# Kernel optimization log

Measured on AMD Instinct MI355X. Metric: run time of the kernel, lower is better.

The kernel has to match this reference:

```python
import jax, jax.numpy as jnp
import numpy as np

D = 28            # matrix_dim = sqrt(word_emb_dim) = sqrt(784)
EMB = D * D       # 784
N_WORDS = 32000


def setup_inputs() -> dict:
    key = jax.random.key(0)
    k1, k2 = jax.random.split(key)
    eye_flat = jnp.eye(D, dtype=jnp.float32).reshape(-1)
    # 'identity' init strategy: N(0, 0.1) + identity on the diagonal
    table = jax.random.normal(k1, (N_WORDS + 1, EMB), dtype=jnp.float32) * 0.1 + eye_flat
    # row 0 is the neutral element (padding) = identity matrix
    table = table.at[0].set(eye_flat)
    sent = jax.random.randint(k2, (2048, 64), 0, N_WORDS + 1, dtype=jnp.int32)
    return {"table": table, "sent": sent}


def reference(table, sent):
    B, S = sent.shape
    # embedding gather -> per-word matrices [B, S, D, D]
    mats = table[sent].reshape(B, S, D, D)
    # continual multiplication: cur = M_0 @ M_1 @ ... @ M_{S-1}
    def step(cur, m):  # cur: [B, D, D], m: [B, D, D]
        return jnp.matmul(cur, m), None
    rest = jnp.moveaxis(mats[:, 1:], 1, 0)  # [S-1, B, D, D]
    out, _ = jax.lax.scan(step, mats[:, 0], rest)
    return out.reshape(B, EMB)
```

## Files before the change

### kernel.cpp

```cpp
#include <hip/hip_runtime.h>
#include <stdint.h>


#define D 28
#define EMB 784
#define SEQ 64
#define NITEMS 2048
#define LPI 7
#define IPW 9
#define RPL 4
#define NCHUNK 28
#define CHUNK_F 256
#define BUF_F (NCHUNK * CHUNK_F)

typedef __attribute__((address_space(3))) uint32_t lds_u32;
typedef const __attribute__((address_space(1))) uint32_t glb_u32;

__device__ __forceinline__ void dma_mat(const float* glane, float* lds0) {
#pragma unroll
  for (int t = 0; t < NCHUNK; ++t)
    __builtin_amdgcn_global_load_lds((glb_u32*)(glane + t * D),
                                     (lds_u32*)(lds0 + t * CHUNK_F), 16, 0, 0);
}

#define MATMUL(Aa, Cc)                                                         \
  do {                                                                         \
    _Pragma("unroll") for (int k = 0; k < D; ++k) {                            \
      _Pragma("unroll") for (int jv = 0; jv < 7; ++jv) {                       \
        float4 m = *(const float4*)(Bs + k * CHUNK_F + 4 * jv);                \
        _Pragma("unroll") for (int r = 0; r < RPL; ++r) {                      \
          float a = Aa[r][k];                                                  \
          if (k == 0) {                                                        \
            Cc[r][4 * jv + 0] = a * m.x;                                       \
            Cc[r][4 * jv + 1] = a * m.y;                                       \
            Cc[r][4 * jv + 2] = a * m.z;                                       \
            Cc[r][4 * jv + 3] = a * m.w;                                       \
          } else {                                                             \
            Cc[r][4 * jv + 0] = fmaf(a, m.x, Cc[r][4 * jv + 0]);               \
            Cc[r][4 * jv + 1] = fmaf(a, m.y, Cc[r][4 * jv + 1]);               \
            Cc[r][4 * jv + 2] = fmaf(a, m.z, Cc[r][4 * jv + 2]);               \
            Cc[r][4 * jv + 3] = fmaf(a, m.w, Cc[r][4 * jv + 3]);               \
          }                                                                    \
        }                                                                      \
      }                                                                        \
    }                                                                          \
  } while (0)

#define STEP(Aa, Cc)                                                           \
  do {                                                                         \
    __builtin_amdgcn_s_waitcnt(0x0f70);           \
    __syncthreads();                                                           \
    MATMUL(Aa, Cc);                                                            \
    __syncthreads();               \
    if (s + 1 < SEG_LEN) {                                                     \
      dma_mat(gn, lds);                                                        \
      int nn = (s + 2 < SEG_LEN) ? s + 2 : SEG_LEN - 1;                        \
      gn = glane(nn);                                                          \
    }                                                                          \
    ++s;                                                                       \
  } while (0)

template <int SEG_LEN, int PSEG, bool GATHER>
__global__ __launch_bounds__(64, 1) void chain_kernel(
    const float* __restrict__ src, const int* __restrict__ sent,
    float* __restrict__ dst, int ntask) {
  __shared__ __align__(16) float lds[BUF_F];

  const int lane = threadIdx.x;
  int slot = lane / LPI;
  int rl = lane - slot * LPI;
  if (slot >= IPW) { slot = IPW - 1; rl = LPI - 1; }
  int task = blockIdx.x * IPW + slot;
  if (task >= ntask) task = ntask - 1;

  const int* sp = nullptr;
  if (GATHER) {
    const int item = task / PSEG;
    const int seg = task - item * PSEG;
    sp = sent + item * SEQ + seg * SEG_LEN;
  }
  auto glane = [&](int s) -> const float* {
    const float* m = GATHER ? src + (size_t)sp[s] * EMB
                            : src + ((size_t)task * SEG_LEN + s) * EMB;
    return m + rl * 4;
  };

  float A0[RPL][D], A1[RPL][D];

  {
    const float* m0 = GATHER ? src + (size_t)sp[0] * EMB
                             : src + (size_t)task * SEG_LEN * EMB;
#pragma unroll
    for (int r = 0; r < RPL; ++r) {
      const float* rp = m0 + (rl * RPL + r) * D;
#pragma unroll
      for (int jv = 0; jv < 7; ++jv) {
        float4 v = *(const float4*)(rp + 4 * jv);
        A0[r][4 * jv + 0] = v.x;
        A0[r][4 * jv + 1] = v.y;
        A0[r][4 * jv + 2] = v.z;
        A0[r][4 * jv + 3] = v.w;
      }
    }
  }

  dma_mat(glane(1), lds);
  const float* gn = glane(SEG_LEN > 2 ? 2 : 1);
  const float* Bs = lds + slot * (LPI * 4);

  int s = 1;
#pragma unroll 1
  for (int p = 0; p < (SEG_LEN - 1) / 2; ++p) {
    STEP(A0, A1);
    STEP(A1, A0);
  }
  STEP(A0, A1);

  {
    float* op = dst + (size_t)task * EMB;
#pragma unroll
    for (int r = 0; r < RPL; ++r) {
      float* rp = op + (rl * RPL + r) * D;
#pragma unroll
      for (int jv = 0; jv < 7; ++jv) {
        *(float4*)(rp + 4 * jv) =
            make_float4(A1[r][4 * jv + 0], A1[r][4 * jv + 1],
                        A1[r][4 * jv + 2], A1[r][4 * jv + 3]);
      }
    }
  }
}

extern "C" void kernel_launch(void* const* d_in, const int* in_sizes, int n_in,
                              void* d_out, int out_size, void* d_ws, size_t ws_size,
                              hipStream_t stream) {
  const float* table = (const float*)d_in[0];
  const int* sent = (const int*)d_in[1];
  float* out = (float*)d_out;

  const size_t need = (size_t)NITEMS * 4 * EMB * sizeof(float);
  if (ws_size >= need) {
    float* p = (float*)d_ws;
    const int ntask1 = NITEMS * 4;
    chain_kernel<16, 4, true><<<(ntask1 + IPW - 1) / IPW, 64, 0, stream>>>(
        table, sent, p, ntask1);
    chain_kernel<4, 1, false><<<(NITEMS + IPW - 1) / IPW, 64, 0, stream>>>(
        p, nullptr, out, NITEMS);
  } else {
    chain_kernel<64, 1, true><<<(NITEMS + IPW - 1) / IPW, 64, 0, stream>>>(
        table, sent, out, NITEMS);
  }
}
```

Baseline: 261.6 us.

## Fuse segment chain and combine stages into one kernel via LDS exchange

Replaces the two-kernel scheme (16-length segment products written to workspace, then a second kernel combining four segments) with one kernel. Each wavefront now handles two items of four segments each (8 slots instead of 9). Segments 1-3 write their partial products into LDS, and slots 0 and 4 multiply them in to produce the final result directly. This removes the workspace round-trip and the second launch, but the full-chain fallback path is dropped, lane 63 is left idle, and most slots sit idle during the final three serial matmuls.

```diff
diff --git a/kernel.cpp b/kernel.cpp
--- a/kernel.cpp
+++ b/kernel.cpp
@@ -7,7 +7,7 @@
 #define SEQ 64
 #define NITEMS 2048
 #define LPI 7
-#define IPW 9
+#define SPW 8
 #define RPL 4
 #define NCHUNK 28
 #define CHUNK_F 256
@@ -60,36 +60,35 @@
     ++s;                                                                       \
   } while (0)
 
-template <int SEG_LEN, int PSEG, bool GATHER>
-__global__ __launch_bounds__(64, 1) void chain_kernel(
+__global__ __launch_bounds__(64, 1) void fused_kernel(
     const float* __restrict__ src, const int* __restrict__ sent,
     float* __restrict__ dst, int ntask) {
+  constexpr int SEG_LEN = 16;
+  constexpr int PSEG = 4;
   __shared__ __align__(16) float lds[BUF_F];
 
   const int lane = threadIdx.x;
   int slot = lane / LPI;
   int rl = lane - slot * LPI;
-  if (slot >= IPW) { slot = IPW - 1; rl = LPI - 1; }
-  int task = blockIdx.x * IPW + slot;
+  if (slot >= SPW) {
+    slot = SPW - 1;
+    rl = (lane - 56 < LPI) ? lane - 56 : LPI - 1;
+  }
+  int task = blockIdx.x * SPW + slot;
   if (task >= ntask) task = ntask - 1;
 
-  const int* sp = nullptr;
-  if (GATHER) {
-    const int item = task / PSEG;
-    const int seg = task - item * PSEG;
-    sp = sent + item * SEQ + seg * SEG_LEN;
-  }
+  const int item = task / PSEG;
+  const int seg = task - item * PSEG;
+  const int* sp = sent + item * SEQ + seg * SEG_LEN;
+
   auto glane = [&](int s) -> const float* {
-    const float* m = GATHER ? src + (size_t)sp[s] * EMB
-                            : src + ((size_t)task * SEG_LEN + s) * EMB;
-    return m + rl * 4;
+    return src + (size_t)sp[s] * EMB + rl * 4;
   };
 
   float A0[RPL][D], A1[RPL][D];
 
   {
-    const float* m0 = GATHER ? src + (size_t)sp[0] * EMB
-                             : src + (size_t)task * SEG_LEN * EMB;
+    const float* m0 = src + (size_t)sp[0] * EMB;
 #pragma unroll
     for (int r = 0; r < RPL; ++r) {
       const float* rp = m0 + (rl * RPL + r) * D;
@@ -105,7 +104,7 @@
   }
 
   dma_mat(glane(1), lds);
-  const float* gn = glane(SEG_LEN > 2 ? 2 : 1);
+  const float* gn = glane(2);
   const float* Bs = lds + slot * (LPI * 4);
 
   int s = 1;
@@ -116,38 +115,63 @@
   }
   STEP(A0, A1);
 
+  __syncthreads();
+
   {
-    float* op = dst + (size_t)task * EMB;
+    const int wslot = (slot >= 4) ? slot - 4 : slot;
+    if (wslot != 0) {
+      const int col = ((slot >= 4) ? 3 : 0) * D + (wslot - 1) * D;
+      float* wp = lds + col;
+#pragma unroll
+      for (int r = 0; r < RPL; ++r) {
+        const int k = rl * RPL + r;
+#pragma unroll
+        for (int jv = 0; jv < 7; ++jv) {
+          *(float4*)(wp + k * CHUNK_F + 4 * jv) =
+              make_float4(A1[r][4 * jv + 0], A1[r][4 * jv + 1],
+                          A1[r][4 * jv + 2], A1[r][4 * jv + 3]);
+        }
+      }
+    }
+  }
+  __syncthreads();
+
+  const int cbase = (slot >= 4) ? 3 * D : 0;
+  {
+    const float* Bs = lds + cbase + 0 * D;
+    MATMUL(A1, A0);
+  }
+  {
+    const float* Bs = lds + cbase + 1 * D;
+    MATMUL(A0, A1);
+  }
+  {
+    const float* Bs = lds + cbase + 2 * D;
+    MATMUL(A1, A0);
+  }
+
+  if (slot == 0 || slot == 4) {
+    float* op = dst + (size_t)item * EMB;
 #pragma unroll
     for (int r = 0; r < RPL; ++r) {
       float* rp = op + (rl * RPL + r) * D;
 #pragma unroll
       for (int jv = 0; jv < 7; ++jv) {
         *(float4*)(rp + 4 * jv) =
-            make_float4(A1[r][4 * jv + 0], A1[r][4 * jv + 1],
-                        A1[r][4 * jv + 2], A1[r][4 * jv + 3]);
+            make_float4(A0[r][4 * jv + 0], A0[r][4 * jv + 1],
+                        A0[r][4 * jv + 2], A0[r][4 * jv + 3]);
       }
     }
   }
 }
 
 extern "C" void kernel_launch(void* const* d_in, const int* in_sizes, int n_in,
-                              void* d_out, int out_size, void* d_ws, size_t ws_size,
-                              hipStream_t stream) {
+                              void* d_out, int out_size, void* d_ws,
+                              size_t ws_size, hipStream_t stream) {
   const float* table = (const float*)d_in[0];
   const int* sent = (const int*)d_in[1];
   float* out = (float*)d_out;
 
-  const size_t need = (size_t)NITEMS * 4 * EMB * sizeof(float);
-  if (ws_size >= need) {
-    float* p = (float*)d_ws;
-    const int ntask1 = NITEMS * 4;
-    chain_kernel<16, 4, true><<<(ntask1 + IPW - 1) / IPW, 64, 0, stream>>>(
-        table, sent, p, ntask1);
-    chain_kernel<4, 1, false><<<(NITEMS + IPW - 1) / IPW, 64, 0, stream>>>(
-        p, nullptr, out, NITEMS);
-  } else {
-    chain_kernel<64, 1, true><<<(NITEMS + IPW - 1) / IPW, 64, 0, stream>>>(
-        table, sent, out, NITEMS);
-  }
+  const int ntask = NITEMS * 4;
+  fused_kernel<<<ntask / SPW, 64, 0, stream>>>(table, sent, out, ntask);
 }
```

Result: faster. 241.9 us (-7.5%).
